# Performance work log

Hardware: AMD Instinct MI355X
Metric: run time of the kernel (lower is better)

## Reference

```python
import jax, jax.numpy as jnp
import numpy as np

B, S, HID = 2, 2048, 2048
H, KV, D = 16, 4, 128          # query heads, kv heads, head_dim
G = H // KV                     # q heads per kv head
RD = 32                         # rotary_dim = int(0.25 * 128), even
THETA = 5000000.0
EPS = 1e-6


def _rms_norm(x, w):
    # out = x * rsqrt(mean(x^2)) * (1 + w)   (weight is zero-init)
    out = x * jax.lax.rsqrt(jnp.mean(x * x, axis=-1, keepdims=True) + EPS)
    return out * (1.0 + w.astype(x.dtype))


def _apply_rope(x, positions):
    # x: [B,S,h,RD]; standard HF rope with rotate_half on the rotary slice
    half = RD // 2
    inv_freq = 1.0 / (THETA ** (jnp.arange(0, half, dtype=jnp.float32) * 2.0 / RD))
    freqs = positions.astype(jnp.float32)[..., None] * inv_freq  # [B,S,half]
    emb = jnp.concatenate([freqs, freqs], axis=-1)               # [B,S,RD]
    cos = jnp.cos(emb)[:, :, None, :].astype(x.dtype)
    sin = jnp.sin(emb)[:, :, None, :].astype(x.dtype)
    x1, x2 = x[..., :half], x[..., half:]
    rot = jnp.concatenate([-x2, x1], axis=-1)
    return x * cos + rot * sin


def _partial_rope(q, k, positions):
    q_rot, q_pass = q[..., :RD], q[..., RD:]
    k_rot, k_pass = k[..., :RD], k[..., RD:]
    q_rot = _apply_rope(q_rot, positions)
    k_rot = _apply_rope(k_rot, positions)
    return (jnp.concatenate([q_rot, q_pass], axis=-1),
            jnp.concatenate([k_rot, k_pass], axis=-1))


def setup_inputs() -> dict:
    k0, k1, k2 = jax.random.split(jax.random.key(0), 3)
    x = jax.random.normal(k0, (B, S, HID), dtype=jnp.float32)
    positions = jnp.broadcast_to(jnp.arange(S, dtype=jnp.int32), (B, S))
    attention_mask = jnp.ones((B, S), dtype=bool)
    wqkv = jax.random.normal(k1, (HID, (H * 2 + 2 * KV) * D), dtype=jnp.float32) * 0.02
    wo = jax.random.normal(k2, (H * D, HID), dtype=jnp.float32) * 0.02
    q_norm_w = jnp.zeros((D,), dtype=jnp.float32)
    k_norm_w = jnp.zeros((D,), dtype=jnp.float32)
    return {"x": x, "positions": positions, "attention_mask": attention_mask,
            "wqkv": wqkv, "wo": wo, "q_norm_w": q_norm_w, "k_norm_w": k_norm_w}


def reference(x, positions, attention_mask, wqkv, wo, q_norm_w, k_norm_w):
    bsz, seq, _ = x.shape
    qkv = jnp.einsum('bsh,hf->bsf', x, wqkv)  # [B,S,5120]
    q_sz, kv_sz = H * 2 * D, KV * D
    q_raw = qkv[..., :q_sz]
    k_raw = qkv[..., q_sz:q_sz + kv_sz]
    v_raw = qkv[..., q_sz + kv_sz:]

    q_all = q_raw.reshape(bsz, seq, H, 2 * D)
    q, gate = jnp.split(q_all, 2, axis=-1)          # each [B,S,H,D]
    gate = gate.reshape(bsz, seq, H * D)

    q = _rms_norm(q, q_norm_w)
    k = _rms_norm(k_raw.reshape(bsz, seq, KV, D), k_norm_w)
    v = v_raw.reshape(bsz, seq, KV, D)
    q, k = _partial_rope(q, k, positions)

    # GQA causal attention, scale = 1/sqrt(head_dim)
    qg = q.reshape(bsz, seq, KV, G, D)
    scores = jnp.einsum('bqkgd,bskd->bkgqs', qg, k) * (1.0 / np.sqrt(D))
    causal = jnp.tril(jnp.ones((seq, seq), dtype=bool))
    mask = causal[None, None, None] & attention_mask[:, None, None, None, :]
    scores = jnp.where(mask, scores, jnp.finfo(scores.dtype).min)
    probs = jax.nn.softmax(scores, axis=-1)
    attn = jnp.einsum('bkgqs,bskd->bqkgd', probs, v)
    attn = attn.reshape(bsz, seq, H * D)

    attn = attn * jax.nn.sigmoid(gate)
    return jnp.einsum('bsf,fh->bsh', attn, wo)
```

## Files before the change

### kernel.cpp

```cpp
#include <hip/hip_runtime.h>

typedef unsigned short u16;
typedef unsigned int u32;
typedef __attribute__((ext_vector_type(8))) short short8;
typedef __attribute__((ext_vector_type(4))) float floatx4;

#define SEQ   2048
#define HIDD  2048
#define NQH   16
#define NKV   4
#define HDIM  128
#define QKV_N 5120
#define K_OFF 4096
#define V_OFF 4608
#define NTOK  4096
#define PSTR  40

__device__ __forceinline__ float b2f(u16 u) {
  u32 x = ((u32)u) << 16;
  return __builtin_bit_cast(float, x);
}
__device__ __forceinline__ u16 f2b(float f) {
  u32 x = __builtin_bit_cast(u32, f);
  u32 r = x + 0x7fffu + ((x >> 16) & 1u);
  return (u16)(r >> 16);
}
__device__ __forceinline__ short8 pack8(floatx4 a, floatx4 b) {
  short8 s;
#pragma unroll
  for (int j = 0; j < 4; j++) { s[j] = (short)f2b(a[j]); s[4 + j] = (short)f2b(b[j]); }
  return s;
}
__device__ __forceinline__ void async_copy16(const u16* g, u16* lds) {
  __builtin_amdgcn_global_load_lds((const __attribute__((address_space(1))) u32*)g,
                                   (__attribute__((address_space(3))) u32*)lds, 16, 0, 0);
}

__global__ __launch_bounds__(256) void cast_bf16(const float* __restrict__ in,
                                                 u16* __restrict__ out, int n8) {
  const int i = blockIdx.x * 256 + threadIdx.x;
  if (i < n8) {
    const floatx4 f0 = *(const floatx4*)(in + (size_t)i * 8);
    const floatx4 f1 = *(const floatx4*)(in + (size_t)i * 8 + 4);
    *(short8*)(out + (size_t)i * 8) = pack8(f0, f1);
  }
}

__global__ __launch_bounds__(256) void transpose_f32_bf16(const float* __restrict__ in,
                                                          u16* __restrict__ out,
                                                          int R, int C) {
  __shared__ float tile[32][33];
  const int bx = blockIdx.x * 32;
  const int by = blockIdx.y * 32;
  const int tx = threadIdx.x & 31;
  const int ty = threadIdx.x >> 5;
#pragma unroll
  for (int i = ty; i < 32; i += 8)
    tile[i][tx] = in[(size_t)(by + i) * C + bx + tx];
  __syncthreads();
#pragma unroll
  for (int i = ty; i < 32; i += 8)
    out[(size_t)(bx + i) * R + by + tx] = f2b(tile[tx][i]);
}

__global__ __launch_bounds__(256) void pack_kv(const u16* __restrict__ qkv,
                                               u16* __restrict__ Kc,
                                               u16* __restrict__ Vp) {
  __shared__ u16 tile[32][136];
  const int t0 = blockIdx.x * 32;
  const int kv = blockIdx.y;
  const int tid = threadIdx.x;
  const int b  = t0 / SEQ;
  const int tl = t0 - b * SEQ;
  const int jt = tl >> 5;
  const size_t kvbase = (size_t)(b * NKV + kv) * SEQ * HDIM;

  const int row  = tid >> 3;
  const int part = tid & 7;
  const size_t qbase = (size_t)(t0 + row) * QKV_N;
  const short8 kv0 = *(const short8*)(qkv + qbase + K_OFF + kv * HDIM + part * 16);
  const short8 kv1 = *(const short8*)(qkv + qbase + K_OFF + kv * HDIM + part * 16 + 8);
  *(short8*)(Kc + kvbase + (size_t)(tl + row) * HDIM + part * 16)     = kv0;
  *(short8*)(Kc + kvbase + (size_t)(tl + row) * HDIM + part * 16 + 8) = kv1;
  const short8 vv0 = *(const short8*)(qkv + qbase + V_OFF + kv * HDIM + part * 16);
  const short8 vv1 = *(const short8*)(qkv + qbase + V_OFF + kv * HDIM + part * 16 + 8);
  *(short8*)&tile[row][part * 16]     = vv0;
  *(short8*)&tile[row][part * 16 + 8] = vv1;
  __syncthreads();
  const int d = tid >> 1;
  const int half = tid & 1;
  u16* vout = Vp + kvbase + (size_t)jt * HDIM * 32 + d * 32 + half * 16;
  short8 o0;
#pragma unroll
  for (int i = 0; i < 8; i++) o0[i] = (short)tile[half * 16 + i][d];
  short8 o1;
#pragma unroll
  for (int i = 0; i < 8; i++) o1[i] = (short)tile[half * 16 + 8 + i][d];
  *(short8*)(vout) = o0;
  *(short8*)(vout + 8) = o1;
}

template <bool C32>
__global__ __launch_bounds__(512, 2) void gemm_bt8(const u16* __restrict__ A,
                                                   const u16* __restrict__ Bt,
                                                   void* __restrict__ Cp,
                                                   int M, int N, int K) {
  __shared__ __align__(16) u16 As[2][256 * 64];
  __shared__ __align__(16) u16 Bs[2][256 * 64];
  const int tid  = threadIdx.x;
  const int wave = tid >> 6;
  const int lane = tid & 63;
  const int lm   = lane & 15;
  const int lq   = lane >> 4;
  const int m0   = blockIdx.y * 256;
  const int n0   = blockIdx.x * 256;
  const int wr   = wave >> 2;
  const int wc   = wave & 3;
  const int NK   = K >> 6;

  const int r0 = wave * 16 + (lane >> 3);
  const int c0 = (((lane & 7) ^ (r0 & 7)) << 3);
  const int dls = wave * 1024;

  auto stageA = [&](int buf, int kt, int h) {
    const u16* g = A + (size_t)(m0 + h * 128 + r0) * K + kt * 64 + c0;
    async_copy16(g,                &As[buf][h * 8192 + dls]);
    async_copy16(g + (size_t)8 * K, &As[buf][h * 8192 + dls + 512]);
  };
  auto stageB = [&](int buf, int kt, int h) {
    const u16* g = Bt + (size_t)(n0 + h * 128 + r0) * K + kt * 64 + c0;
    async_copy16(g,                &Bs[buf][h * 8192 + dls]);
    async_copy16(g + (size_t)8 * K, &Bs[buf][h * 8192 + dls + 512]);
  };
  auto rdA = [&](int buf, int row, int ch) {
    return *(const short8*)&As[buf][row * 64 + ((ch ^ (row & 7)) << 3)];
  };
  auto rdB = [&](int buf, int row, int ch) {
    return *(const short8*)&Bs[buf][row * 64 + ((ch ^ (row & 7)) << 3)];
  };

  floatx4 acc[8][4] = {};
  short8 aF[4][2], bF[4][2];

  stageA(0, 0, 0); stageA(0, 0, 1);
  stageB(0, 0, 0); stageB(0, 0, 1);
  stageB(1, 1, 0); stageB(1, 1, 1);
  asm volatile("s_waitcnt vmcnt(4)" ::: "memory");
  __builtin_amdgcn_sched_barrier(0);
  __builtin_amdgcn_s_barrier();

  for (int j = 0; j < NK; ++j) {
    const int cur = j & 1;
#pragma unroll
    for (int m = 0; m < 4; ++m)
#pragma unroll
      for (int kk = 0; kk < 2; ++kk)
        aF[m][kk] = rdA(cur, wr * 128 + m * 16 + lm, kk * 4 + lq);
#pragma unroll
    for (int n = 0; n < 2; ++n)
#pragma unroll
      for (int kk = 0; kk < 2; ++kk)
        bF[n][kk] = rdB(cur, wc * 64 + n * 16 + lm, kk * 4 + lq);
    if (j + 1 < NK) stageA(cur ^ 1, j + 1, 0);
    __builtin_amdgcn_s_barrier();
    asm volatile("s_waitcnt lgkmcnt(0)" ::: "memory");
    __builtin_amdgcn_sched_barrier(0);
    __builtin_amdgcn_s_setprio(1);
#pragma unroll
    for (int m = 0; m < 4; ++m)
#pragma unroll
      for (int n = 0; n < 2; ++n)
#pragma unroll
        for (int kk = 0; kk < 2; ++kk)
          acc[m][n] = __builtin_amdgcn_mfma_f32_16x16x32_bf16(aF[m][kk], bF[n][kk], acc[m][n], 0, 0, 0);
    __builtin_amdgcn_s_setprio(0);
    __builtin_amdgcn_s_barrier();
#pragma unroll
    for (int n = 0; n < 2; ++n)
#pragma unroll
      for (int kk = 0; kk < 2; ++kk)
        bF[2 + n][kk] = rdB(cur, wc * 64 + (2 + n) * 16 + lm, kk * 4 + lq);
    if (j + 1 < NK) stageA(cur ^ 1, j + 1, 1);
    __builtin_amdgcn_s_barrier();
    asm volatile("s_waitcnt lgkmcnt(0)" ::: "memory");
    __builtin_amdgcn_sched_barrier(0);
    __builtin_amdgcn_s_setprio(1);
#pragma unroll
    for (int m = 0; m < 4; ++m)
#pragma unroll
      for (int n = 0; n < 2; ++n)
#pragma unroll
        for (int kk = 0; kk < 2; ++kk)
          acc[m][2 + n] = __builtin_amdgcn_mfma_f32_16x16x32_bf16(aF[m][kk], bF[2 + n][kk], acc[m][2 + n], 0, 0, 0);
    __builtin_amdgcn_s_setprio(0);
    __builtin_amdgcn_s_barrier();
#pragma unroll
    for (int m = 0; m < 4; ++m)
#pragma unroll
      for (int kk = 0; kk < 2; ++kk)
        aF[m][kk] = rdA(cur, wr * 128 + 64 + m * 16 + lm, kk * 4 + lq);
    if (j + 2 < NK) stageB(cur, j + 2, 0);
    __builtin_amdgcn_s_barrier();
    asm volatile("s_waitcnt lgkmcnt(0)" ::: "memory");
    __builtin_amdgcn_sched_barrier(0);
    __builtin_amdgcn_s_setprio(1);
#pragma unroll
    for (int m = 0; m < 4; ++m)
#pragma unroll
      for (int n = 0; n < 2; ++n)
#pragma unroll
        for (int kk = 0; kk < 2; ++kk)
          acc[4 + m][n] = __builtin_amdgcn_mfma_f32_16x16x32_bf16(aF[m][kk], bF[n][kk], acc[4 + m][n], 0, 0, 0);
    __builtin_amdgcn_s_setprio(0);
    __builtin_amdgcn_s_barrier();
    if (j + 2 < NK) stageB(cur, j + 2, 1);
    __builtin_amdgcn_s_barrier();
    __builtin_amdgcn_s_setprio(1);
#pragma unroll
    for (int m = 0; m < 4; ++m)
#pragma unroll
      for (int n = 0; n < 2; ++n)
#pragma unroll
        for (int kk = 0; kk < 2; ++kk)
          acc[4 + m][2 + n] = __builtin_amdgcn_mfma_f32_16x16x32_bf16(aF[m][kk], bF[2 + n][kk], acc[4 + m][2 + n], 0, 0, 0);
    __builtin_amdgcn_s_setprio(0);
    if (j + 2 < NK) asm volatile("s_waitcnt vmcnt(4)" ::: "memory");
    else            asm volatile("s_waitcnt vmcnt(0)" ::: "memory");
    __builtin_amdgcn_sched_barrier(0);
    __builtin_amdgcn_s_barrier();
  }

#pragma unroll
  for (int mi = 0; mi < 8; ++mi)
#pragma unroll
    for (int ni = 0; ni < 4; ++ni)
#pragma unroll
      for (int r = 0; r < 4; ++r) {
        const int row = m0 + wr * 128 + mi * 16 + lq * 4 + r;
        const int col = n0 + wc * 64 + ni * 16 + lm;
        if (C32) ((float*)Cp)[(size_t)row * N + col] = acc[mi][ni][r];
        else     ((u16*)Cp)[(size_t)row * N + col] = f2b(acc[mi][ni][r]);
      }
}

__global__ __launch_bounds__(64) void postproc(u16* __restrict__ qkv,
                                               const int* __restrict__ positions,
                                               const float* __restrict__ qw,
                                               const float* __restrict__ kw) {
  const int tok  = blockIdx.x;
  const int u    = blockIdx.y;
  const int lane = threadIdx.x;
  const float* w;
  int base;
  if (u < NQH) { base = u * 256; w = qw; }
  else         { base = K_OFF + (u - NQH) * HDIM; w = kw; }
  u16* p = qkv + (size_t)tok * QKV_N + base;
  const int d0 = lane * 2;
  float v0 = b2f(p[d0]);
  float v1 = b2f(p[d0 + 1]);
  float ss = v0 * v0 + v1 * v1;
#pragma unroll
  for (int off = 32; off >= 1; off >>= 1) ss += __shfl_xor(ss, off, 64);
  const float rs = rsqrtf(ss * (1.0f / 128.0f) + 1e-6f);
  v0 = v0 * rs * (1.0f + w[d0]);
  v1 = v1 * rs * (1.0f + w[d0 + 1]);
  const float pv0 = __shfl_xor(v0, 8, 64);
  const float pv1 = __shfl_xor(v1, 8, 64);
  if (d0 < 32) {
    const float fpos = (float)positions[tok];
    const int i = d0 & 15;
    const float inv0 = __powf(5.0e6f, -((float)i) / 16.0f);
    const float inv1 = __powf(5.0e6f, -((float)(i + 1)) / 16.0f);
    float s0, c0, s1, c1;
    sincosf(fpos * inv0, &s0, &c0);
    sincosf(fpos * inv1, &s1, &c1);
    if (d0 < 16) { v0 = v0 * c0 - pv0 * s0; v1 = v1 * c1 - pv1 * s1; }
    else         { v0 = v0 * c0 + pv0 * s0; v1 = v1 * c1 + pv1 * s1; }
  }
  if (u < NQH) {
    v0 *= 0.08838834764831845f;
    v1 *= 0.08838834764831845f;
  }
  p[d0]     = f2b(v0);
  p[d0 + 1] = f2b(v1);
}

__global__ __launch_bounds__(256) void attn_kernel(const u16* __restrict__ qkv,
                                                   const u16* __restrict__ Kc,
                                                   const u16* __restrict__ Vp,
                                                   u16* __restrict__ attn_g) {
  __shared__ __align__(16) u16 Ks[2][4][32][32];
  __shared__ __align__(16) u16 Vs[2][128][32];
  __shared__ __align__(16) u16 P_lds[4][16 * PSTR];
  const int tid  = threadIdx.x;
  const int wave = tid >> 6;
  const int lane = tid & 63;
  const int lm = lane & 15;
  const int lq = lane >> 4;
  const int kvi = blockIdx.y;
  const int b   = blockIdx.z;
  const int h   = kvi * 4 + wave;
  const size_t tokbase = (size_t)b * SEQ;
  const size_t kvbase  = (size_t)(b * NKV + kvi) * SEQ * HDIM;
  const int klocal = lane >> 2;
  const int kpart  = (lane & 3) * 8;

  short8 onesF;
#pragma unroll
  for (int j = 0; j < 8; j++) onesF[j] = (short)0x3F80;

  auto stage = [&](int buf, int j) {
    const u16* ksrc = Kc + kvbase + (size_t)j * 32 * HDIM;
#pragma unroll
    for (int half = 0; half < 2; half++)
      async_copy16(ksrc + (size_t)(half * 16 + klocal) * HDIM + wave * 32 + kpart,
                   &Ks[buf][wave][half * 16][0]);
    const u16* vsrc = Vp + kvbase + (size_t)j * (HDIM * 32);
#pragma unroll
    for (int i = 0; i < 2; i++)
      async_copy16(vsrc + wave * 1024 + i * 512 + lane * 8,
                   &Vs[buf][wave * 32 + i * 16][0]);
  };

  auto run_tile = [&](int t) {
    short8 qF[4];
    const u16* qp = qkv + (tokbase + 16 * t + lm) * QKV_N + h * 256;
#pragma unroll
    for (int kc = 0; kc < 4; kc++)
      qF[kc] = *(const short8*)(qp + kc * 32 + lq * 8);

    floatx4 O[8] = {};
    floatx4 lacc = {};
    const int jmax = t >> 1;
    const int moff = (t & 1) * 16;

    __syncthreads();
    stage(0, 0);
    for (int j = 0; j <= jmax; j++) {
      const int cur = j & 1;
      __syncthreads();
      if (j < jmax) stage(cur ^ 1, j + 1);
      short8 kF[2][4], vF[8];
#pragma unroll
      for (int n0 = 0; n0 < 2; n0++)
#pragma unroll
        for (int kc = 0; kc < 4; kc++)
          kF[n0][kc] = *(const short8*)&Ks[cur][kc][n0 * 16 + lm][lq * 8];
#pragma unroll
      for (int dc = 0; dc < 8; dc++)
        vF[dc] = *(const short8*)&Vs[cur][dc * 16 + lm][lq * 8];

      floatx4 Sc[2] = {};
#pragma unroll
      for (int n0 = 0; n0 < 2; n0++)
#pragma unroll
        for (int kc = 0; kc < 4; kc++)
          Sc[n0] = __builtin_amdgcn_mfma_f32_16x16x32_bf16(qF[kc], kF[n0][kc], Sc[n0], 0, 0, 0);

      const bool masked = (j == jmax);
#pragma unroll
      for (int n0 = 0; n0 < 2; n0++)
#pragma unroll
        for (int r = 0; r < 4; r++) {
          float pe = __expf(Sc[n0][r]);
          if (masked) {
            const int rowloc = lq * 4 + r;
            const int keyloc = n0 * 16 + lm;
            pe = (keyloc <= rowloc + moff) ? pe : 0.0f;
          }
          P_lds[wave][(lq * 4 + r) * PSTR + n0 * 16 + lm] = f2b(pe);
        }
      const short8 pF = *(const short8*)&P_lds[wave][lm * PSTR + lq * 8];
      lacc = __builtin_amdgcn_mfma_f32_16x16x32_bf16(pF, onesF, lacc, 0, 0, 0);
#pragma unroll
      for (int dc = 0; dc < 8; dc++)
        O[dc] = __builtin_amdgcn_mfma_f32_16x16x32_bf16(pF, vF[dc], O[dc], 0, 0, 0);
    }

#pragma unroll
    for (int r = 0; r < 4; r++) {
      const int row = 16 * t + lq * 4 + r;
      const size_t tok = tokbase + row;
      const float inv_l = 1.0f / lacc[r];
#pragma unroll
      for (int dc = 0; dc < 8; dc++) {
        const int d = dc * 16 + lm;
        const float g = b2f(qkv[tok * QKV_N + h * 256 + 128 + d]);
        const float sg = 1.0f / (1.0f + __expf(-g));
        attn_g[tok * HIDD + h * HDIM + d] = f2b(O[dc][r] * inv_l * sg);
      }
    }
  };

  const int p = blockIdx.x;
  run_tile(p);
  run_tile(127 - p);
}

extern "C" void kernel_launch(void* const* d_in, const int* in_sizes, int n_in,
                              void* d_out, int out_size, void* d_ws, size_t ws_size,
                              hipStream_t stream) {
  const float* x        = (const float*)d_in[0];
  const int* positions  = (const int*)d_in[1];
  const float* wqkv     = (const float*)d_in[3];
  const float* wo       = (const float*)d_in[4];
  const float* qnw      = (const float*)d_in[5];
  const float* knw      = (const float*)d_in[6];
  float* out = (float*)d_out;

  char* ws = (char*)d_ws;
  u16* qkv    = (u16*)(ws);
  u16* wqkv_t = (u16*)(ws + 41943040);
  u16* attn_g = (u16*)(ws + 41943040);
  u16* Kc     = (u16*)(ws + 58720256);
  u16* wo_t   = (u16*)(ws);
  u16* xb     = (u16*)d_out;
  u16* Vp     = (u16*)d_out;

  cast_bf16<<<dim3(NTOK * HIDD / 8 / 256), 256, 0, stream>>>(x, xb, NTOK * HIDD / 8);
  transpose_f32_bf16<<<dim3(QKV_N / 32, HIDD / 32), 256, 0, stream>>>(wqkv, wqkv_t, HIDD, QKV_N);
  gemm_bt8<false><<<dim3(QKV_N / 256, NTOK / 256), 512, 0, stream>>>(xb, wqkv_t, qkv, NTOK, QKV_N, HIDD);
  postproc<<<dim3(NTOK, NQH + NKV), 64, 0, stream>>>(qkv, positions, qnw, knw);
  pack_kv<<<dim3(NTOK / 32, NKV), 256, 0, stream>>>(qkv, Kc, Vp);
  attn_kernel<<<dim3(64, NKV, 2), 256, 0, stream>>>(qkv, Kc, Vp, attn_g);
  transpose_f32_bf16<<<dim3(HIDD / 32, HIDD / 32), 256, 0, stream>>>(wo, wo_t, HIDD, HIDD);
  gemm_bt8<true><<<dim3(HIDD / 256, NTOK / 256), 512, 0, stream>>>(attn_g, wo_t, out, NTOK, HIDD, HIDD);
}
```

Before: 452.6 us.

## Remap GEMM blocks across XCDs, add 256x128 output GEMM, swizzle attention LDS

The GEMM block index is remapped so that consecutive tiles are grouped per XCD (bid&7 chunks), which aims to improve L2 locality. A new 256x128-tile GEMM variant is used for the output projection, doubling the block count from 128 to 256 so all CUs on the chip get work. The attention kernel's K/V LDS staging and reads now use an XOR swizzle to reduce LDS bank conflicts. The smaller N tile lowers per-block reuse of A, and the swizzle has to stay consistent between writes and reads.

```diff
diff --git a/kernel.cpp b/kernel.cpp
--- a/kernel.cpp
+++ b/kernel.cpp
@@ -112,8 +112,11 @@
   const int lane = tid & 63;
   const int lm   = lane & 15;
   const int lq   = lane >> 4;
-  const int m0   = blockIdx.y * 256;
-  const int n0   = blockIdx.x * 256;
+  const int nwg = gridDim.x * gridDim.y;
+  const int bid = blockIdx.y * gridDim.x + blockIdx.x;
+  const int sbid = (bid & 7) * (nwg >> 3) + (bid >> 3);
+  const int m0   = (sbid / gridDim.x) * 256;
+  const int n0   = (sbid % gridDim.x) * 256;
   const int wr   = wave >> 2;
   const int wc   = wave & 3;
   const int NK   = K >> 6;
@@ -237,6 +240,117 @@
 #pragma unroll
       for (int r = 0; r < 4; ++r) {
         const int row = m0 + wr * 128 + mi * 16 + lq * 4 + r;
+        const int col = n0 + wc * 64 + ni * 16 + lm;
+        if (C32) ((float*)Cp)[(size_t)row * N + col] = acc[mi][ni][r];
+        else     ((u16*)Cp)[(size_t)row * N + col] = f2b(acc[mi][ni][r]);
+      }
+}
+
+template <bool C32>
+__global__ __launch_bounds__(512, 2) void gemm_n128(const u16* __restrict__ A,
+                                                    const u16* __restrict__ Bt,
+                                                    void* __restrict__ Cp,
+                                                    int M, int N, int K) {
+  __shared__ __align__(16) u16 As[2][256 * 64];
+  __shared__ __align__(16) u16 Bs[2][128 * 64];
+  const int tid  = threadIdx.x;
+  const int wave = tid >> 6;
+  const int lane = tid & 63;
+  const int lm   = lane & 15;
+  const int lq   = lane >> 4;
+  const int nwg = gridDim.x * gridDim.y;
+  const int bid = blockIdx.y * gridDim.x + blockIdx.x;
+  const int sbid = (bid & 7) * (nwg >> 3) + (bid >> 3);
+  const int m0   = (sbid / gridDim.x) * 256;
+  const int n0   = (sbid % gridDim.x) * 128;
+  const int wr   = wave >> 1;
+  const int wc   = wave & 1;
+  const int NK   = K >> 6;
+
+  auto stA = [&](int buf, int kt, int L) {
+    const int cd  = L * 512 + wave * 64 + lane;
+    const int row = cd >> 3;
+    const int ch  = cd & 7;
+    async_copy16(A + (size_t)(m0 + row) * K + kt * 64 + ((ch ^ (row & 7)) << 3),
+                 &As[buf][(L * 512 + wave * 64) * 8]);
+  };
+  auto stB = [&](int buf, int kt, int L) {
+    const int cd  = L * 512 + wave * 64 + lane;
+    const int row = cd >> 3;
+    const int ch  = cd & 7;
+    async_copy16(Bt + (size_t)(n0 + row) * K + kt * 64 + ((ch ^ (row & 7)) << 3),
+                 &Bs[buf][(L * 512 + wave * 64) * 8]);
+  };
+  auto rdA = [&](int buf, int row, int ch) {
+    return *(const short8*)&As[buf][row * 64 + ((ch ^ (row & 7)) << 3)];
+  };
+  auto rdB = [&](int buf, int row, int ch) {
+    return *(const short8*)&Bs[buf][row * 64 + ((ch ^ (row & 7)) << 3)];
+  };
+
+  floatx4 acc[4][4] = {};
+  short8 aF[4][2], bF[4][2];
+
+  stA(0, 0, 0); stA(0, 0, 1); stA(0, 0, 2); stA(0, 0, 3);
+  stB(0, 0, 0); stB(0, 0, 1);
+  stB(1, 1, 0); stB(1, 1, 1);
+  asm volatile("s_waitcnt vmcnt(2)" ::: "memory");
+  __builtin_amdgcn_sched_barrier(0);
+  __builtin_amdgcn_s_barrier();
+
+  for (int j = 0; j < NK; ++j) {
+    const int cur = j & 1;
+#pragma unroll
+    for (int m = 0; m < 4; ++m)
+#pragma unroll
+      for (int kk = 0; kk < 2; ++kk)
+        aF[m][kk] = rdA(cur, wr * 64 + m * 16 + lm, kk * 4 + lq);
+#pragma unroll
+    for (int n = 0; n < 4; ++n)
+#pragma unroll
+      for (int kk = 0; kk < 2; ++kk)
+        bF[n][kk] = rdB(cur, wc * 64 + n * 16 + lm, kk * 4 + lq);
+    if (j + 1 < NK) { stA(cur ^ 1, j + 1, 0); stA(cur ^ 1, j + 1, 1); }
+    asm volatile("s_waitcnt lgkmcnt(8)" ::: "memory");
+    __builtin_amdgcn_s_barrier();
+    asm volatile("s_waitcnt lgkmcnt(0)" ::: "memory");
+    __builtin_amdgcn_sched_barrier(0);
+    __builtin_amdgcn_s_setprio(1);
+#pragma unroll
+    for (int m = 0; m < 4; ++m)
+#pragma unroll
+      for (int n = 0; n < 2; ++n)
+#pragma unroll
+        for (int kk = 0; kk < 2; ++kk)
+          acc[m][n] = __builtin_amdgcn_mfma_f32_16x16x32_bf16(aF[m][kk], bF[n][kk], acc[m][n], 0, 0, 0);
+    __builtin_amdgcn_s_setprio(0);
+    __builtin_amdgcn_s_barrier();
+    if (j + 1 < NK) { stA(cur ^ 1, j + 1, 2); stA(cur ^ 1, j + 1, 3); }
+    if (j + 2 < NK) { stB(cur, j + 2, 0); stB(cur, j + 2, 1); }
+    __builtin_amdgcn_s_barrier();
+    __builtin_amdgcn_sched_barrier(0);
+    __builtin_amdgcn_s_setprio(1);
+#pragma unroll
+    for (int m = 0; m < 4; ++m)
+#pragma unroll
+      for (int n = 0; n < 2; ++n)
+#pragma unroll
+        for (int kk = 0; kk < 2; ++kk)
+          acc[m][2 + n] = __builtin_amdgcn_mfma_f32_16x16x32_bf16(aF[m][kk], bF[2 + n][kk], acc[m][2 + n], 0, 0, 0);
+    __builtin_amdgcn_s_setprio(0);
+    if (j + 2 < NK) asm volatile("s_waitcnt vmcnt(2)" ::: "memory");
+    else            asm volatile("s_waitcnt vmcnt(0)" ::: "memory");
+    __builtin_amdgcn_sched_barrier(0);
+    __builtin_amdgcn_s_barrier();
+  }
+
+#pragma unroll
+  for (int mi = 0; mi < 4; ++mi)
+#pragma unroll
+    for (int ni = 0; ni < 4; ++ni)
+#pragma unroll
+      for (int r = 0; r < 4; ++r) {
+        const int row = m0 + wr * 64 + mi * 16 + lq * 4 + r;
         const int col = n0 + wc * 64 + ni * 16 + lm;
         if (C32) ((float*)Cp)[(size_t)row * N + col] = acc[mi][ni][r];
         else     ((u16*)Cp)[(size_t)row * N + col] = f2b(acc[mi][ni][r]);
@@ -303,7 +417,8 @@
   const size_t tokbase = (size_t)b * SEQ;
   const size_t kvbase  = (size_t)(b * NKV + kvi) * SEQ * HDIM;
   const int klocal = lane >> 2;
-  const int kpart  = (lane & 3) * 8;
+  const int ssw = ((lane & 3) ^ ((lane >> 3) & 3)) * 8;
+  const int rsw = (lq ^ ((lm >> 1) & 3)) * 8;
 
   short8 onesF;
 #pragma unroll
@@ -313,12 +428,12 @@
     const u16* ksrc = Kc + kvbase + (size_t)j * 32 * HDIM;
 #pragma unroll
     for (int half = 0; half < 2; half++)
-      async_copy16(ksrc + (size_t)(half * 16 + klocal) * HDIM + wave * 32 + kpart,
+      async_copy16(ksrc + (size_t)(half * 16 + klocal) * HDIM + wave * 32 + ssw,
                    &Ks[buf][wave][half * 16][0]);
     const u16* vsrc = Vp + kvbase + (size_t)j * (HDIM * 32);
 #pragma unroll
     for (int i = 0; i < 2; i++)
-      async_copy16(vsrc + wave * 1024 + i * 512 + lane * 8,
+      async_copy16(vsrc + wave * 1024 + i * 512 + (lane >> 2) * 32 + ssw,
                    &Vs[buf][wave * 32 + i * 16][0]);
   };
 
@@ -345,10 +460,10 @@
       for (int n0 = 0; n0 < 2; n0++)
 #pragma unroll
         for (int kc = 0; kc < 4; kc++)
-          kF[n0][kc] = *(const short8*)&Ks[cur][kc][n0 * 16 + lm][lq * 8];
+          kF[n0][kc] = *(const short8*)&Ks[cur][kc][n0 * 16 + lm][rsw];
 #pragma unroll
       for (int dc = 0; dc < 8; dc++)
-        vF[dc] = *(const short8*)&Vs[cur][dc * 16 + lm][lq * 8];
+        vF[dc] = *(const short8*)&Vs[cur][dc * 16 + lm][rsw];
 
       floatx4 Sc[2] = {};
 #pragma unroll
@@ -424,5 +539,5 @@
   pack_kv<<<dim3(NTOK / 32, NKV), 256, 0, stream>>>(qkv, Kc, Vp);
   attn_kernel<<<dim3(64, NKV, 2), 256, 0, stream>>>(qkv, Kc, Vp, attn_g);
   transpose_f32_bf16<<<dim3(HIDD / 32, HIDD / 32), 256, 0, stream>>>(wo, wo_t, HIDD, HIDD);
-  gemm_bt8<true><<<dim3(HIDD / 256, NTOK / 256), 512, 0, stream>>>(attn_g, wo_t, out, NTOK, HIDD, HIDD);
-}
+  gemm_n128<true><<<dim3(HIDD / 128, NTOK / 256), 512, 0, stream>>>(attn_g, wo_t, out, NTOK, HIDD, HIDD);
+}
```

After: 432.7 us. 1.05x faster.
